# Optimization experiments

Measured on AMD Instinct MI355X. Metric: run time of the kernel, lower is better.

## Reference

```python
import jax, jax.numpy as jnp
import numpy as np
import math

IN_FEATURES = 4096
OUT_FEATURES = 4096
TOKENS = 8192


def hadamard(x):
    """Orthonormal fast Walsh-Hadamard transform along last dim (power of two)."""
    n = x.shape[-1]
    orig_shape = x.shape
    y = x.reshape(-1, n)
    h = 1
    while h < n:  # log2(n) butterfly steps (static loop, n known at trace time)
        y = y.reshape(-1, n // (2 * h), 2 * h)
        left = y[..., :h]
        right = y[..., h:2 * h]
        y = jnp.concatenate([left + right, left - right], axis=-1)
        y = y.reshape(-1, n)
        h *= 2
    return (y / math.sqrt(n)).reshape(orig_shape)


def setup_inputs() -> dict:
    key = jax.random.key(0)
    k1, k2, k3, k4 = jax.random.split(key, 4)
    x = jax.random.normal(k1, (TOKENS, IN_FEATURES), dtype=jnp.float32)
    # int8-valued quantized weights, stored as int32 for portability
    Q_tilde = jax.random.randint(k2, (OUT_FEATURES, IN_FEATURES), -127, 128, dtype=jnp.int32)
    # per-row scales, positive, realistic magnitude (~max_abs/127)
    s_tilde = jax.random.uniform(k3, (OUT_FEATURES, 1), dtype=jnp.float32, minval=0.001, maxval=0.02)
    bias = jax.random.normal(k4, (OUT_FEATURES,), dtype=jnp.float32)
    return {"x": x, "Q_tilde": Q_tilde, "s_tilde": s_tilde, "bias": bias}


def reference(x, Q_tilde, s_tilde, bias):
    # y = hadamard(x) @ (Q * s)^T + bias
    xh = hadamard(x)                                      # [T, in]
    W = Q_tilde.astype(jnp.float32) * s_tilde             # [out, in] dequantized
    y = xh @ W.T + bias                                   # [T, out]
    return y
```

## Files before the change

### kernel.cpp

```cpp
#include <hip/hip_runtime.h>
#include <hip/hip_bf16.h>

typedef int   i32x4 __attribute__((ext_vector_type(4)));
typedef unsigned int   u32;
typedef unsigned short u16;
typedef signed char    i8;

#define TOKENS 8192
#define NDIM   4096
#define KDIM   4096
#define BK     64
#define NKT    (KDIM / BK)

__global__ __launch_bounds__(64)
void fwht_rows_q8(const float* __restrict__ x, i8* __restrict__ xq,
                  float* __restrict__ xscale) {
  const int row = blockIdx.x;
  const int l   = threadIdx.x;

  const float4* xv = reinterpret_cast<const float4*>(x + (size_t)row * KDIM) + l * 16;
  float v[64];
#pragma unroll
  for (int j = 0; j < 16; ++j) {
    float4 f = xv[j];
    v[4*j+0] = f.x; v[4*j+1] = f.y; v[4*j+2] = f.z; v[4*j+3] = f.w;
  }

#pragma unroll
  for (int h = 1; h < 64; h <<= 1) {
#pragma unroll
    for (int j = 0; j < 64; ++j) {
      if ((j & h) == 0) {
        float a = v[j], b = v[j + h];
        v[j] = a + b; v[j + h] = a - b;
      }
    }
  }

#pragma unroll
  for (int m = 1; m < 64; m <<= 1) {
    const bool up = (l & m) != 0;
#pragma unroll
    for (int j = 0; j < 64; ++j) {
      float p = __shfl_xor(v[j], m, 64);
      v[j] = up ? (p - v[j]) : (v[j] + p);
    }
  }

  float mxu = 0.f;
#pragma unroll
  for (int j = 0; j < 64; ++j) mxu = fmaxf(mxu, fabsf(v[j]));
#pragma unroll
  for (int m = 1; m < 64; m <<= 1) mxu = fmaxf(mxu, __shfl_xor(mxu, m, 64));
  mxu = fmaxf(mxu, 1e-30f);
  const float inv = 127.0f / mxu;

  i8* orow = xq + (size_t)row * KDIM + l * 64;
#pragma unroll
  for (int g = 0; g < 4; ++g) {
    u32 w[4];
#pragma unroll
    for (int q4 = 0; q4 < 4; ++q4) {
      int b0 = __float2int_rn(v[g*16+q4*4+0] * inv);
      int b1 = __float2int_rn(v[g*16+q4*4+1] * inv);
      int b2 = __float2int_rn(v[g*16+q4*4+2] * inv);
      int b3 = __float2int_rn(v[g*16+q4*4+3] * inv);
      b0 = min(127, max(-127, b0)); b1 = min(127, max(-127, b1));
      b2 = min(127, max(-127, b2)); b3 = min(127, max(-127, b3));
      w[q4] = (u32)(b0 & 0xff) | ((u32)(b1 & 0xff) << 8) |
              ((u32)(b2 & 0xff) << 16) | ((u32)(b3 & 0xff) << 24);
    }
    uint4 pk; pk.x = w[0]; pk.y = w[1]; pk.z = w[2]; pk.w = w[3];
    *reinterpret_cast<uint4*>(orow + g * 16) = pk;
  }
  if (l == 0) xscale[row] = mxu * (0.015625f / 127.0f);
}

__device__ __forceinline__ u32 pack4(int4 q) {
  return (u32)(q.x & 0xff) | ((u32)(q.y & 0xff) << 8) |
         ((u32)(q.z & 0xff) << 16) | ((u32)(q.w & 0xff) << 24);
}
__global__ __launch_bounds__(256)
void qpack(const int* __restrict__ Q, i8* __restrict__ W8) {
  const size_t idx = ((size_t)blockIdx.x * 256 + threadIdx.x) * 16;
  int4 a = *reinterpret_cast<const int4*>(Q + idx);
  int4 b = *reinterpret_cast<const int4*>(Q + idx + 4);
  int4 c = *reinterpret_cast<const int4*>(Q + idx + 8);
  int4 d = *reinterpret_cast<const int4*>(Q + idx + 12);
  uint4 pk; pk.x = pack4(a); pk.y = pack4(b); pk.z = pack4(c); pk.w = pack4(d);
  *reinterpret_cast<uint4*>(W8 + idx) = pk;
}

__global__ __launch_bounds__(512, 4)
void gemm_i8_2b(const i8* __restrict__ A, const i8* __restrict__ B,
                const float* __restrict__ xscale, const float* __restrict__ s,
                const float* __restrict__ bias, float* __restrict__ C) {
  __shared__ __align__(16) i8 lds[2 * 24576];

  const int th   = threadIdx.x;
  const int wave = th >> 6;
  const int lane = th & 63;

  const int b0 = blockIdx.x;
  const int xc = b0 & 7;
  const int i  = b0 >> 3;
  const int mt = i >> 2;
  const int nt = xc * 4 + (i & 3);

  const int srow = th >> 2;
  const int scol = ((th & 3) * 16) ^ (((th >> 5) & 1) << 5);
  const i8* gA0 = A + (size_t)(mt * 256 + srow) * KDIM + scol;
  const i8* gA1 = gA0 + (size_t)128 * KDIM;
  const i8* gB0 = B + (size_t)(nt * 128 + srow) * KDIM + scol;

  const int ldsA0 = wave * 1024;
  const int ldsA1 = 8192 + wave * 1024;
  const int ldsB0 = 16384 + wave * 1024;

#define STAGE(tt, ss) do {                                                      \
    __builtin_amdgcn_global_load_lds(                                           \
      (const __attribute__((address_space(1))) void*)(gA0 + (size_t)(tt) * BK), \
      (__attribute__((address_space(3))) void*)(lds + (ss) * 24576 + ldsA0), 16, 0, 0); \
    __builtin_amdgcn_global_load_lds(                                           \
      (const __attribute__((address_space(1))) void*)(gA1 + (size_t)(tt) * BK), \
      (__attribute__((address_space(3))) void*)(lds + (ss) * 24576 + ldsA1), 16, 0, 0); \
    __builtin_amdgcn_global_load_lds(                                           \
      (const __attribute__((address_space(1))) void*)(gB0 + (size_t)(tt) * BK), \
      (__attribute__((address_space(3))) void*)(lds + (ss) * 24576 + ldsB0), 16, 0, 0); \
  } while (0)

  const int wm = wave >> 1;
  const int wn = wave & 1;
  const int laneRow = lane & 15;
  const int kByte   = (lane >> 4) << 4;
  const int swz     = ((lane >> 3) & 1) << 5;
  const int aOff = (((wm * 64 + laneRow) * 64 + kByte) ^ swz);
  const int bOff = (((wn * 64 + laneRow) * 64 + kByte) ^ swz) + 16384;

  i32x4 acc[4][4];
#pragma unroll
  for (int mi = 0; mi < 4; ++mi)
#pragma unroll
    for (int ni = 0; ni < 4; ++ni)
      acc[mi][ni] = i32x4{0, 0, 0, 0};

  STAGE(0, 0);
  asm volatile("s_waitcnt vmcnt(0)" ::: "memory");
  __builtin_amdgcn_s_barrier();

  for (int t = 0; t < NKT; ++t) {
    const char* cur = (const char*)lds + (t & 1) * 24576;
    if (t + 1 < NKT) STAGE(t + 1, (t + 1) & 1);

    i32x4 bfr[4], af[4];
#pragma unroll
    for (int ni = 0; ni < 4; ++ni)
      bfr[ni] = *(const i32x4*)(cur + bOff + ni * 1024);
#pragma unroll
    for (int mi = 0; mi < 4; ++mi)
      af[mi] = *(const i32x4*)(cur + aOff + mi * 1024);

    __builtin_amdgcn_s_setprio(1);
#pragma unroll
    for (int mi = 0; mi < 4; ++mi)
#pragma unroll
      for (int ni = 0; ni < 4; ++ni)
        acc[mi][ni] = __builtin_amdgcn_mfma_i32_16x16x64_i8(af[mi], bfr[ni], acc[mi][ni], 0, 0, 0);
    __builtin_amdgcn_s_setprio(0);

    asm volatile("s_waitcnt vmcnt(0)" ::: "memory");
    __builtin_amdgcn_s_barrier();
  }
#undef STAGE

  const int col0 = nt * 128 + wn * 64 + (lane & 15);
  const int row0 = mt * 256 + wm * 64 + ((lane >> 4) << 2);
  float xs[4][4];
#pragma unroll
  for (int mi = 0; mi < 4; ++mi)
#pragma unroll
    for (int r = 0; r < 4; ++r)
      xs[r][mi] = xscale[row0 + mi * 16 + r];
#pragma unroll
  for (int ni = 0; ni < 4; ++ni) {
    const float sc = s[col0 + ni * 16];
    const float bv = bias[col0 + ni * 16];
#pragma unroll
    for (int mi = 0; mi < 4; ++mi) {
      float* cp = C + (size_t)(row0 + mi * 16) * NDIM + col0 + ni * 16;
#pragma unroll
      for (int r = 0; r < 4; ++r)
        cp[(size_t)r * NDIM] = (float)acc[mi][ni][r] * (xs[r][mi] * sc) + bv;
    }
  }
}

extern "C" void kernel_launch(void* const* d_in, const int* in_sizes, int n_in,
                              void* d_out, int out_size, void* d_ws, size_t ws_size,
                              hipStream_t stream) {
  (void)in_sizes; (void)n_in; (void)out_size; (void)ws_size;
  const float* x    = (const float*)d_in[0];
  const int*   Q    = (const int*)d_in[1];
  const float* s    = (const float*)d_in[2];
  const float* bias = (const float*)d_in[3];
  float* out = (float*)d_out;

  i8*    xq     = (i8*)d_ws;
  i8*    W8     = xq + (size_t)TOKENS * KDIM;
  float* xscale = (float*)(W8 + (size_t)NDIM * KDIM);

  fwht_rows_q8<<<dim3(TOKENS), dim3(64), 0, stream>>>(x, xq, xscale);
  qpack<<<dim3((NDIM * KDIM) / (256 * 16)), dim3(256), 0, stream>>>(Q, W8);
  gemm_i8_2b<<<dim3((TOKENS / 256) * (NDIM / 128)), dim3(512), 0, stream>>>(
      xq, W8, xscale, s, bias, out);
}
```

Measured before the change: 219.4 us.

## Replace LDS-staged int8 GEMM with direct-to-register double-buffered loads on 256x256 tiles

The GEMM no longer stages tiles through shared memory. Each wave loads its A and B MFMA fragments straight from global memory into registers, using two register sets so the next K-step loads while the current one computes, and the kernel has no barriers. The block tile grows from 256x128 to 256x256 and each wave owns a 128x64 sub-tile, which raises register use and lowers the occupancy hint to 2. The cost is the loss of LDS data sharing between waves: each fragment is now fetched from global/L2 by several waves, and the per-lane 16-byte strided row loads may coalesce poorly.

Result: slower. 460.2 us (+109.8%).

```diff
diff --git a/kernel.cpp b/kernel.cpp
--- a/kernel.cpp
+++ b/kernel.cpp
@@ -91,12 +91,10 @@
   *reinterpret_cast<uint4*>(W8 + idx) = pk;
 }
 
-__global__ __launch_bounds__(512, 4)
-void gemm_i8_2b(const i8* __restrict__ A, const i8* __restrict__ B,
+__global__ __launch_bounds__(512, 2)
+void gemm_dr_i8(const i8* __restrict__ A, const i8* __restrict__ B,
                 const float* __restrict__ xscale, const float* __restrict__ s,
                 const float* __restrict__ bias, float* __restrict__ C) {
-  __shared__ __align__(16) i8 lds[2 * 24576];
-
   const int th   = threadIdx.x;
   const int wave = th >> 6;
   const int lane = th & 63;
@@ -104,80 +102,73 @@
   const int b0 = blockIdx.x;
   const int xc = b0 & 7;
   const int i  = b0 >> 3;
-  const int mt = i >> 2;
-  const int nt = xc * 4 + (i & 3);
-
-  const int srow = th >> 2;
-  const int scol = ((th & 3) * 16) ^ (((th >> 5) & 1) << 5);
-  const i8* gA0 = A + (size_t)(mt * 256 + srow) * KDIM + scol;
-  const i8* gA1 = gA0 + (size_t)128 * KDIM;
-  const i8* gB0 = B + (size_t)(nt * 128 + srow) * KDIM + scol;
-
-  const int ldsA0 = wave * 1024;
-  const int ldsA1 = 8192 + wave * 1024;
-  const int ldsB0 = 16384 + wave * 1024;
-
-#define STAGE(tt, ss) do {                                                      \
-    __builtin_amdgcn_global_load_lds(                                           \
-      (const __attribute__((address_space(1))) void*)(gA0 + (size_t)(tt) * BK), \
-      (__attribute__((address_space(3))) void*)(lds + (ss) * 24576 + ldsA0), 16, 0, 0); \
-    __builtin_amdgcn_global_load_lds(                                           \
-      (const __attribute__((address_space(1))) void*)(gA1 + (size_t)(tt) * BK), \
-      (__attribute__((address_space(3))) void*)(lds + (ss) * 24576 + ldsA1), 16, 0, 0); \
-    __builtin_amdgcn_global_load_lds(                                           \
-      (const __attribute__((address_space(1))) void*)(gB0 + (size_t)(tt) * BK), \
-      (__attribute__((address_space(3))) void*)(lds + (ss) * 24576 + ldsB0), 16, 0, 0); \
-  } while (0)
-
-  const int wm = wave >> 1;
-  const int wn = wave & 1;
+  const int mt = i >> 1;
+  const int nt = xc * 2 + (i & 1);
+
+  const int wm = wave >> 2;
+  const int wn = wave & 3;
   const int laneRow = lane & 15;
-  const int kByte   = (lane >> 4) << 4;
-  const int swz     = ((lane >> 3) & 1) << 5;
-  const int aOff = (((wm * 64 + laneRow) * 64 + kByte) ^ swz);
-  const int bOff = (((wn * 64 + laneRow) * 64 + kByte) ^ swz) + 16384;
-
-  i32x4 acc[4][4];
-#pragma unroll
-  for (int mi = 0; mi < 4; ++mi)
+  const int kB      = (lane >> 4) << 4;
+
+  u32 aoff[8], boff[4];
+#pragma unroll
+  for (int mi = 0; mi < 8; ++mi)
+    aoff[mi] = (u32)(mt * 256 + wm * 128 + mi * 16 + laneRow) * (u32)KDIM + (u32)kB;
+#pragma unroll
+  for (int ni = 0; ni < 4; ++ni)
+    boff[ni] = (u32)(nt * 256 + wn * 64 + ni * 16 + laneRow) * (u32)KDIM + (u32)kB;
+
+  i32x4 acc[8][4];
+#pragma unroll
+  for (int mi = 0; mi < 8; ++mi)
 #pragma unroll
     for (int ni = 0; ni < 4; ++ni)
       acc[mi][ni] = i32x4{0, 0, 0, 0};
 
-  STAGE(0, 0);
+  i32x4 a0[8], b0f[4], a1[8], b1f[4];
+
+#define LOADSET(as, bs, tt) do {                                        \
+    _Pragma("unroll")                                                   \
+    for (int mi = 0; mi < 8; ++mi)                                      \
+      as[mi] = *(const i32x4*)(A + aoff[mi] + (tt) * BK);               \
+    _Pragma("unroll")                                                   \
+    for (int ni = 0; ni < 4; ++ni)                                      \
+      bs[ni] = *(const i32x4*)(B + boff[ni] + (tt) * BK);               \
+  } while (0)
+
+#define MFMASET(as, bs) do {                                            \
+    _Pragma("unroll")                                                   \
+    for (int mi = 0; mi < 8; ++mi)                                      \
+      _Pragma("unroll")                                                 \
+      for (int ni = 0; ni < 4; ++ni)                                    \
+        acc[mi][ni] = __builtin_amdgcn_mfma_i32_16x16x64_i8(            \
+            as[mi], bs[ni], acc[mi][ni], 0, 0, 0);                      \
+  } while (0)
+
+  LOADSET(a0, b0f, 0);
+  LOADSET(a1, b1f, 1);
+
+  for (int t = 0; t < NKT - 2; t += 2) {
+    asm volatile("s_waitcnt vmcnt(12)" ::: "memory");
+    MFMASET(a0, b0f);
+    LOADSET(a0, b0f, t + 2);
+    asm volatile("s_waitcnt vmcnt(12)" ::: "memory");
+    MFMASET(a1, b1f);
+    LOADSET(a1, b1f, t + 3);
+  }
+  asm volatile("s_waitcnt vmcnt(12)" ::: "memory");
+  MFMASET(a0, b0f);
   asm volatile("s_waitcnt vmcnt(0)" ::: "memory");
-  __builtin_amdgcn_s_barrier();
-
-  for (int t = 0; t < NKT; ++t) {
-    const char* cur = (const char*)lds + (t & 1) * 24576;
-    if (t + 1 < NKT) STAGE(t + 1, (t + 1) & 1);
-
-    i32x4 bfr[4], af[4];
-#pragma unroll
-    for (int ni = 0; ni < 4; ++ni)
-      bfr[ni] = *(const i32x4*)(cur + bOff + ni * 1024);
-#pragma unroll
-    for (int mi = 0; mi < 4; ++mi)
-      af[mi] = *(const i32x4*)(cur + aOff + mi * 1024);
-
-    __builtin_amdgcn_s_setprio(1);
-#pragma unroll
-    for (int mi = 0; mi < 4; ++mi)
-#pragma unroll
-      for (int ni = 0; ni < 4; ++ni)
-        acc[mi][ni] = __builtin_amdgcn_mfma_i32_16x16x64_i8(af[mi], bfr[ni], acc[mi][ni], 0, 0, 0);
-    __builtin_amdgcn_s_setprio(0);
-
-    asm volatile("s_waitcnt vmcnt(0)" ::: "memory");
-    __builtin_amdgcn_s_barrier();
-  }
-#undef STAGE
-
-  const int col0 = nt * 128 + wn * 64 + (lane & 15);
-  const int row0 = mt * 256 + wm * 64 + ((lane >> 4) << 2);
-  float xs[4][4];
-#pragma unroll
-  for (int mi = 0; mi < 4; ++mi)
+  MFMASET(a1, b1f);
+
+#undef LOADSET
+#undef MFMASET
+
+  const int col0 = nt * 256 + wn * 64 + (lane & 15);
+  const int row0 = mt * 256 + wm * 128 + ((lane >> 4) << 2);
+  float xs[4][8];
+#pragma unroll
+  for (int mi = 0; mi < 8; ++mi)
 #pragma unroll
     for (int r = 0; r < 4; ++r)
       xs[r][mi] = xscale[row0 + mi * 16 + r];
@@ -186,7 +177,7 @@
     const float sc = s[col0 + ni * 16];
     const float bv = bias[col0 + ni * 16];
 #pragma unroll
-    for (int mi = 0; mi < 4; ++mi) {
+    for (int mi = 0; mi < 8; ++mi) {
       float* cp = C + (size_t)(row0 + mi * 16) * NDIM + col0 + ni * 16;
 #pragma unroll
       for (int r = 0; r < 4; ++r)
@@ -211,6 +202,6 @@
 
   fwht_rows_q8<<<dim3(TOKENS), dim3(64), 0, stream>>>(x, xq, xscale);
   qpack<<<dim3((NDIM * KDIM) / (256 * 16)), dim3(256), 0, stream>>>(Q, W8);
-  gemm_i8_2b<<<dim3((TOKENS / 256) * (NDIM / 128)), dim3(512), 0, stream>>>(
+  gemm_dr_i8<<<dim3((TOKENS / 256) * (NDIM / 256)), dim3(512), 0, stream>>>(
       xq, W8, xscale, s, bias, out);
 }
```

## Enlarge GEMM tile to 256x256 with triple-buffered LDS and fuse prep kernels

Applied to the files above, without the earlier changes.

The int8 GEMM moves from a 256x128 tile with 8 waves to a 256x256 tile with 4 waves. Each wave now holds an 8x8 grid of MFMA accumulators, and the K loop uses a three-slot LDS ring that prefetches two tiles ahead, with hand-placed waitcnt and sched barriers so LDS fragment loads overlap MFMAs. The FWHT/quantize and weight-pack kernels are merged into one launch to cut launch overhead. This raises arithmetic intensity and reduces barriers per MFMA, but heavy register pressure (256 accumulator registers) limits occupancy to one block per SIMD group and risks spills.

New measurement: 426.6 us. 94.5% more time.

```diff
diff --git a/kernel.cpp b/kernel.cpp
--- a/kernel.cpp
+++ b/kernel.cpp
@@ -11,12 +11,29 @@
 #define KDIM   4096
 #define BK     64
 #define NKT    (KDIM / BK)
-
-__global__ __launch_bounds__(64)
-void fwht_rows_q8(const float* __restrict__ x, i8* __restrict__ xq,
-                  float* __restrict__ xscale) {
-  const int row = blockIdx.x;
-  const int l   = threadIdx.x;
+#define SLOT   32768
+
+__device__ __forceinline__ u32 pack4(int4 q) {
+  return (u32)(q.x & 0xff) | ((u32)(q.y & 0xff) << 8) |
+         ((u32)(q.z & 0xff) << 16) | ((u32)(q.w & 0xff) << 24);
+}
+
+__global__ __launch_bounds__(256)
+void fused_aux(const float* __restrict__ x, i8* __restrict__ xq,
+               float* __restrict__ xscale,
+               const int* __restrict__ Q, i8* __restrict__ W8) {
+  if (blockIdx.x >= 2048) {
+    const size_t idx = (((size_t)(blockIdx.x - 2048)) * 256 + threadIdx.x) * 16;
+    int4 a = *reinterpret_cast<const int4*>(Q + idx);
+    int4 b = *reinterpret_cast<const int4*>(Q + idx + 4);
+    int4 c = *reinterpret_cast<const int4*>(Q + idx + 8);
+    int4 d = *reinterpret_cast<const int4*>(Q + idx + 12);
+    uint4 pk; pk.x = pack4(a); pk.y = pack4(b); pk.z = pack4(c); pk.w = pack4(d);
+    *reinterpret_cast<uint4*>(W8 + idx) = pk;
+    return;
+  }
+  const int row = blockIdx.x * 4 + (threadIdx.x >> 6);
+  const int l   = threadIdx.x & 63;
 
   const float4* xv = reinterpret_cast<const float4*>(x + (size_t)row * KDIM) + l * 16;
   float v[64];
@@ -76,26 +93,11 @@
   if (l == 0) xscale[row] = mxu * (0.015625f / 127.0f);
 }
 
-__device__ __forceinline__ u32 pack4(int4 q) {
-  return (u32)(q.x & 0xff) | ((u32)(q.y & 0xff) << 8) |
-         ((u32)(q.z & 0xff) << 16) | ((u32)(q.w & 0xff) << 24);
-}
-__global__ __launch_bounds__(256)
-void qpack(const int* __restrict__ Q, i8* __restrict__ W8) {
-  const size_t idx = ((size_t)blockIdx.x * 256 + threadIdx.x) * 16;
-  int4 a = *reinterpret_cast<const int4*>(Q + idx);
-  int4 b = *reinterpret_cast<const int4*>(Q + idx + 4);
-  int4 c = *reinterpret_cast<const int4*>(Q + idx + 8);
-  int4 d = *reinterpret_cast<const int4*>(Q + idx + 12);
-  uint4 pk; pk.x = pack4(a); pk.y = pack4(b); pk.z = pack4(c); pk.w = pack4(d);
-  *reinterpret_cast<uint4*>(W8 + idx) = pk;
-}
-
-__global__ __launch_bounds__(512, 4)
-void gemm_i8_2b(const i8* __restrict__ A, const i8* __restrict__ B,
-                const float* __restrict__ xscale, const float* __restrict__ s,
-                const float* __restrict__ bias, float* __restrict__ C) {
-  __shared__ __align__(16) i8 lds[2 * 24576];
+__global__ __launch_bounds__(256, 1)
+void gemm_w4(const i8* __restrict__ A, const i8* __restrict__ B,
+             const float* __restrict__ xscale, const float* __restrict__ s,
+             const float* __restrict__ bias, float* __restrict__ C) {
+  __shared__ __align__(16) i8 lds[3 * SLOT];
 
   const int th   = threadIdx.x;
   const int wave = th >> 6;
@@ -104,29 +106,30 @@
   const int b0 = blockIdx.x;
   const int xc = b0 & 7;
   const int i  = b0 >> 3;
-  const int mt = i >> 2;
-  const int nt = xc * 4 + (i & 3);
+  const int mt = i >> 1;
+  const int nt = xc * 2 + (i & 1);
 
   const int srow = th >> 2;
   const int scol = ((th & 3) * 16) ^ (((th >> 5) & 1) << 5);
-  const i8* gA0 = A + (size_t)(mt * 256 + srow) * KDIM + scol;
-  const i8* gA1 = gA0 + (size_t)128 * KDIM;
-  const i8* gB0 = B + (size_t)(nt * 128 + srow) * KDIM + scol;
-
-  const int ldsA0 = wave * 1024;
-  const int ldsA1 = 8192 + wave * 1024;
-  const int ldsB0 = 16384 + wave * 1024;
-
-#define STAGE(tt, ss) do {                                                      \
-    __builtin_amdgcn_global_load_lds(                                           \
-      (const __attribute__((address_space(1))) void*)(gA0 + (size_t)(tt) * BK), \
-      (__attribute__((address_space(3))) void*)(lds + (ss) * 24576 + ldsA0), 16, 0, 0); \
-    __builtin_amdgcn_global_load_lds(                                           \
-      (const __attribute__((address_space(1))) void*)(gA1 + (size_t)(tt) * BK), \
-      (__attribute__((address_space(3))) void*)(lds + (ss) * 24576 + ldsA1), 16, 0, 0); \
-    __builtin_amdgcn_global_load_lds(                                           \
-      (const __attribute__((address_space(1))) void*)(gB0 + (size_t)(tt) * BK), \
-      (__attribute__((address_space(3))) void*)(lds + (ss) * 24576 + ldsB0), 16, 0, 0); \
+  const i8* gA[4]; const i8* gB[4];
+#pragma unroll
+  for (int j = 0; j < 4; ++j) {
+    gA[j] = A + (size_t)(mt * 256 + j * 64 + srow) * KDIM + scol;
+    gB[j] = B + (size_t)(nt * 256 + j * 64 + srow) * KDIM + scol;
+  }
+  const int ldsW = wave * 1024;
+
+#define STAGE(tt, ss) do {                                                        \
+    _Pragma("unroll")                                                             \
+    for (int j = 0; j < 4; ++j)                                                   \
+      __builtin_amdgcn_global_load_lds(                                           \
+        (const __attribute__((address_space(1))) void*)(gA[j] + (size_t)(tt) * BK), \
+        (__attribute__((address_space(3))) void*)(lds + (ss) * SLOT + j * 4096 + ldsW), 16, 0, 0); \
+    _Pragma("unroll")                                                             \
+    for (int j = 0; j < 4; ++j)                                                   \
+      __builtin_amdgcn_global_load_lds(                                           \
+        (const __attribute__((address_space(1))) void*)(gB[j] + (size_t)(tt) * BK), \
+        (__attribute__((address_space(3))) void*)(lds + (ss) * SLOT + 16384 + j * 4096 + ldsW), 16, 0, 0); \
   } while (0)
 
   const int wm = wave >> 1;
@@ -134,59 +137,101 @@
   const int laneRow = lane & 15;
   const int kByte   = (lane >> 4) << 4;
   const int swz     = ((lane >> 3) & 1) << 5;
-  const int aOff = (((wm * 64 + laneRow) * 64 + kByte) ^ swz);
-  const int bOff = (((wn * 64 + laneRow) * 64 + kByte) ^ swz) + 16384;
-
-  i32x4 acc[4][4];
-#pragma unroll
-  for (int mi = 0; mi < 4; ++mi)
-#pragma unroll
-    for (int ni = 0; ni < 4; ++ni)
+  const int aOff = (((wm * 128 + laneRow) * 64 + kByte) ^ swz);
+  const int bOff = (((wn * 128 + laneRow) * 64 + kByte) ^ swz) + 16384;
+
+  i32x4 acc[8][8];
+#pragma unroll
+  for (int mi = 0; mi < 8; ++mi)
+#pragma unroll
+    for (int ni = 0; ni < 8; ++ni)
       acc[mi][ni] = i32x4{0, 0, 0, 0};
 
+  i32x4 afA[4], afB[4], bf0[8], bf1[8];
+
   STAGE(0, 0);
-  asm volatile("s_waitcnt vmcnt(0)" ::: "memory");
+  STAGE(1, 1);
+  asm volatile("s_waitcnt vmcnt(8)" ::: "memory");
+  __builtin_amdgcn_sched_barrier(0);
   __builtin_amdgcn_s_barrier();
-
-  for (int t = 0; t < NKT; ++t) {
-    const char* cur = (const char*)lds + (t & 1) * 24576;
-    if (t + 1 < NKT) STAGE(t + 1, (t + 1) & 1);
-
-    i32x4 bfr[4], af[4];
-#pragma unroll
-    for (int ni = 0; ni < 4; ++ni)
-      bfr[ni] = *(const i32x4*)(cur + bOff + ni * 1024);
+  {
+    const char* c0 = (const char*)lds;
+#pragma unroll
+    for (int ni = 0; ni < 8; ++ni)
+      bf0[ni] = *(const i32x4*)(c0 + bOff + ni * 1024);
 #pragma unroll
     for (int mi = 0; mi < 4; ++mi)
-      af[mi] = *(const i32x4*)(cur + aOff + mi * 1024);
-
-    __builtin_amdgcn_s_setprio(1);
-#pragma unroll
-    for (int mi = 0; mi < 4; ++mi)
-#pragma unroll
-      for (int ni = 0; ni < 4; ++ni)
-        acc[mi][ni] = __builtin_amdgcn_mfma_i32_16x16x64_i8(af[mi], bfr[ni], acc[mi][ni], 0, 0, 0);
-    __builtin_amdgcn_s_setprio(0);
-
-    asm volatile("s_waitcnt vmcnt(0)" ::: "memory");
-    __builtin_amdgcn_s_barrier();
-  }
+      afA[mi] = *(const i32x4*)(c0 + aOff + mi * 1024);
+  }
+
+  int sCur = 0, sNxt = 1, sStg = 2;
+
+#define TILE(t, BFC, BFN) do {                                                    \
+    const char* cur = (const char*)lds + sCur * SLOT;                             \
+    const char* nxt = (const char*)lds + sNxt * SLOT;                             \
+    _Pragma("unroll")                                                             \
+    for (int mi = 0; mi < 4; ++mi)                                                \
+      afB[mi] = *(const i32x4*)(cur + aOff + 4096 + mi * 1024);                   \
+    if ((t) + 2 < NKT) STAGE((t) + 2, sStg);                                      \
+    asm volatile("s_waitcnt lgkmcnt(4)" ::: "memory");       \
+    __builtin_amdgcn_sched_barrier(0);                                            \
+    __builtin_amdgcn_s_setprio(1);                                                \
+    _Pragma("unroll")                                                             \
+    for (int mi = 0; mi < 4; ++mi)                                                \
+      _Pragma("unroll")                                                           \
+      for (int ni = 0; ni < 8; ++ni)                                              \
+        acc[mi][ni] = __builtin_amdgcn_mfma_i32_16x16x64_i8(afA[mi], BFC[ni],     \
+                                                            acc[mi][ni], 0, 0, 0); \
+    __builtin_amdgcn_s_setprio(0);                                                \
+    if ((t) + 2 < NKT)      { asm volatile("s_waitcnt vmcnt(8)" ::: "memory"); }  \
+    else if ((t) + 1 < NKT) { asm volatile("s_waitcnt vmcnt(0)" ::: "memory"); }  \
+    __builtin_amdgcn_sched_barrier(0);                                            \
+    if ((t) + 1 < NKT) {                                                          \
+      __builtin_amdgcn_s_barrier();      \
+      _Pragma("unroll")                                                           \
+      for (int ni = 0; ni < 8; ++ni)                                              \
+        BFN[ni] = *(const i32x4*)(nxt + bOff + ni * 1024);                        \
+      _Pragma("unroll")                                                           \
+      for (int mi = 0; mi < 4; ++mi)                                              \
+        afA[mi] = *(const i32x4*)(nxt + aOff + mi * 1024);                        \
+      asm volatile("s_waitcnt lgkmcnt(12)" ::: "memory");          \
+      __builtin_amdgcn_sched_barrier(0);                                          \
+    } else {                                                                      \
+      asm volatile("s_waitcnt lgkmcnt(0)" ::: "memory");                          \
+      __builtin_amdgcn_sched_barrier(0);                                          \
+    }                                                                             \
+    __builtin_amdgcn_s_setprio(1);                                                \
+    _Pragma("unroll")                                                             \
+    for (int mi = 0; mi < 4; ++mi)                                                \
+      _Pragma("unroll")                                                           \
+      for (int ni = 0; ni < 8; ++ni)                                              \
+        acc[mi + 4][ni] = __builtin_amdgcn_mfma_i32_16x16x64_i8(afB[mi], BFC[ni], \
+                                                        acc[mi + 4][ni], 0, 0, 0); \
+    __builtin_amdgcn_s_setprio(0);                                                \
+    int _tmp = sCur; sCur = sNxt; sNxt = sStg; sStg = _tmp;                       \
+  } while (0)
+
+  for (int t = 0; t < NKT; t += 2) {
+    TILE(t,     bf0, bf1);
+    TILE(t + 1, bf1, bf0);
+  }
+#undef TILE
 #undef STAGE
 
-  const int col0 = nt * 128 + wn * 64 + (lane & 15);
-  const int row0 = mt * 256 + wm * 64 + ((lane >> 4) << 2);
-  float xs[4][4];
-#pragma unroll
-  for (int mi = 0; mi < 4; ++mi)
+  const int col0 = nt * 256 + wn * 128 + (lane & 15);
+  const int row0 = mt * 256 + wm * 128 + ((lane >> 4) << 2);
+  float xs[4][8];
+#pragma unroll
+  for (int mi = 0; mi < 8; ++mi)
 #pragma unroll
     for (int r = 0; r < 4; ++r)
       xs[r][mi] = xscale[row0 + mi * 16 + r];
 #pragma unroll
-  for (int ni = 0; ni < 4; ++ni) {
+  for (int ni = 0; ni < 8; ++ni) {
     const float sc = s[col0 + ni * 16];
     const float bv = bias[col0 + ni * 16];
 #pragma unroll
-    for (int mi = 0; mi < 4; ++mi) {
+    for (int mi = 0; mi < 8; ++mi) {
       float* cp = C + (size_t)(row0 + mi * 16) * NDIM + col0 + ni * 16;
 #pragma unroll
       for (int r = 0; r < 4; ++r)
@@ -209,8 +254,7 @@
   i8*    W8     = xq + (size_t)TOKENS * KDIM;
   float* xscale = (float*)(W8 + (size_t)NDIM * KDIM);
 
-  fwht_rows_q8<<<dim3(TOKENS), dim3(64), 0, stream>>>(x, xq, xscale);
-  qpack<<<dim3((NDIM * KDIM) / (256 * 16)), dim3(256), 0, stream>>>(Q, W8);
-  gemm_i8_2b<<<dim3((TOKENS / 256) * (NDIM / 128)), dim3(512), 0, stream>>>(
+  fused_aux<<<dim3(6144), dim3(256), 0, stream>>>(x, xq, xscale, Q, W8);
+  gemm_w4<<<dim3((TOKENS / 256) * (NDIM / 256)), dim3(256), 0, stream>>>(
       xq, W8, xscale, s, bias, out);
 }
```

## Fuse FWHT and weight packing into one launch; use 4-wave GEMM with 128x64 wave tiles

Applied to the files above, without the earlier changes.

The FWHT-quantize and int32-to-int8 weight packing kernels become one launch, with block ranges split by blockIdx, and the FWHT packs four rows into each 256-thread block. The GEMM keeps its 256x128 block tile but drops from 8 waves to 4. Each wave now computes a 128x64 sub-tile with 8x4 MFMA accumulators, which raises register reuse of the B fragments and cuts LDS reads per MFMA. The cost is higher register pressure (launch bounds 256,2), fewer waves to hide latency, and more global-to-LDS loads per thread per stage.

After: 201.8 us. 1.09x faster.

```diff
diff --git a/kernel.cpp b/kernel.cpp
--- a/kernel.cpp
+++ b/kernel.cpp
@@ -11,12 +11,29 @@
 #define KDIM   4096
 #define BK     64
 #define NKT    (KDIM / BK)
-
-__global__ __launch_bounds__(64)
-void fwht_rows_q8(const float* __restrict__ x, i8* __restrict__ xq,
-                  float* __restrict__ xscale) {
-  const int row = blockIdx.x;
-  const int l   = threadIdx.x;
+#define SLOT   24576
+
+__device__ __forceinline__ u32 pack4(int4 q) {
+  return (u32)(q.x & 0xff) | ((u32)(q.y & 0xff) << 8) |
+         ((u32)(q.z & 0xff) << 16) | ((u32)(q.w & 0xff) << 24);
+}
+
+__global__ __launch_bounds__(256)
+void fused_aux(const float* __restrict__ x, i8* __restrict__ xq,
+               float* __restrict__ xscale,
+               const int* __restrict__ Q, i8* __restrict__ W8) {
+  if (blockIdx.x >= 2048) {
+    const size_t idx = (((size_t)(blockIdx.x - 2048)) * 256 + threadIdx.x) * 16;
+    int4 a = *reinterpret_cast<const int4*>(Q + idx);
+    int4 b = *reinterpret_cast<const int4*>(Q + idx + 4);
+    int4 c = *reinterpret_cast<const int4*>(Q + idx + 8);
+    int4 d = *reinterpret_cast<const int4*>(Q + idx + 12);
+    uint4 pk; pk.x = pack4(a); pk.y = pack4(b); pk.z = pack4(c); pk.w = pack4(d);
+    *reinterpret_cast<uint4*>(W8 + idx) = pk;
+    return;
+  }
+  const int row = blockIdx.x * 4 + (threadIdx.x >> 6);
+  const int l   = threadIdx.x & 63;
 
   const float4* xv = reinterpret_cast<const float4*>(x + (size_t)row * KDIM) + l * 16;
   float v[64];
@@ -76,26 +93,11 @@
   if (l == 0) xscale[row] = mxu * (0.015625f / 127.0f);
 }
 
-__device__ __forceinline__ u32 pack4(int4 q) {
-  return (u32)(q.x & 0xff) | ((u32)(q.y & 0xff) << 8) |
-         ((u32)(q.z & 0xff) << 16) | ((u32)(q.w & 0xff) << 24);
-}
-__global__ __launch_bounds__(256)
-void qpack(const int* __restrict__ Q, i8* __restrict__ W8) {
-  const size_t idx = ((size_t)blockIdx.x * 256 + threadIdx.x) * 16;
-  int4 a = *reinterpret_cast<const int4*>(Q + idx);
-  int4 b = *reinterpret_cast<const int4*>(Q + idx + 4);
-  int4 c = *reinterpret_cast<const int4*>(Q + idx + 8);
-  int4 d = *reinterpret_cast<const int4*>(Q + idx + 12);
-  uint4 pk; pk.x = pack4(a); pk.y = pack4(b); pk.z = pack4(c); pk.w = pack4(d);
-  *reinterpret_cast<uint4*>(W8 + idx) = pk;
-}
-
-__global__ __launch_bounds__(512, 4)
-void gemm_i8_2b(const i8* __restrict__ A, const i8* __restrict__ B,
-                const float* __restrict__ xscale, const float* __restrict__ s,
-                const float* __restrict__ bias, float* __restrict__ C) {
-  __shared__ __align__(16) i8 lds[2 * 24576];
+__global__ __launch_bounds__(256, 2)
+void gemm_2x4(const i8* __restrict__ A, const i8* __restrict__ B,
+              const float* __restrict__ xscale, const float* __restrict__ s,
+              const float* __restrict__ bias, float* __restrict__ C) {
+  __shared__ __align__(16) i8 lds[2 * SLOT];
 
   const int th   = threadIdx.x;
   const int wave = th >> 6;
@@ -109,24 +111,26 @@
 
   const int srow = th >> 2;
   const int scol = ((th & 3) * 16) ^ (((th >> 5) & 1) << 5);
-  const i8* gA0 = A + (size_t)(mt * 256 + srow) * KDIM + scol;
-  const i8* gA1 = gA0 + (size_t)128 * KDIM;
-  const i8* gB0 = B + (size_t)(nt * 128 + srow) * KDIM + scol;
-
-  const int ldsA0 = wave * 1024;
-  const int ldsA1 = 8192 + wave * 1024;
-  const int ldsB0 = 16384 + wave * 1024;
-
-#define STAGE(tt, ss) do {                                                      \
-    __builtin_amdgcn_global_load_lds(                                           \
-      (const __attribute__((address_space(1))) void*)(gA0 + (size_t)(tt) * BK), \
-      (__attribute__((address_space(3))) void*)(lds + (ss) * 24576 + ldsA0), 16, 0, 0); \
-    __builtin_amdgcn_global_load_lds(                                           \
-      (const __attribute__((address_space(1))) void*)(gA1 + (size_t)(tt) * BK), \
-      (__attribute__((address_space(3))) void*)(lds + (ss) * 24576 + ldsA1), 16, 0, 0); \
-    __builtin_amdgcn_global_load_lds(                                           \
-      (const __attribute__((address_space(1))) void*)(gB0 + (size_t)(tt) * BK), \
-      (__attribute__((address_space(3))) void*)(lds + (ss) * 24576 + ldsB0), 16, 0, 0); \
+  const i8* gA[4]; const i8* gB[2];
+#pragma unroll
+  for (int j = 0; j < 4; ++j)
+    gA[j] = A + (size_t)(mt * 256 + j * 64 + srow) * KDIM + scol;
+#pragma unroll
+  for (int j = 0; j < 2; ++j)
+    gB[j] = B + (size_t)(nt * 128 + j * 64 + srow) * KDIM + scol;
+  const int ldsW = wave * 1024;
+
+#define STAGE(tt, ss) do {                                                        \
+    _Pragma("unroll")                                                             \
+    for (int j = 0; j < 4; ++j)                                                   \
+      __builtin_amdgcn_global_load_lds(                                           \
+        (const __attribute__((address_space(1))) void*)(gA[j] + (size_t)(tt) * BK), \
+        (__attribute__((address_space(3))) void*)(lds + (ss) * SLOT + j * 4096 + ldsW), 16, 0, 0); \
+    _Pragma("unroll")                                                             \
+    for (int j = 0; j < 2; ++j)                                                   \
+      __builtin_amdgcn_global_load_lds(                                           \
+        (const __attribute__((address_space(1))) void*)(gB[j] + (size_t)(tt) * BK), \
+        (__attribute__((address_space(3))) void*)(lds + (ss) * SLOT + 16384 + j * 4096 + ldsW), 16, 0, 0); \
   } while (0)
 
   const int wm = wave >> 1;
@@ -134,12 +138,12 @@
   const int laneRow = lane & 15;
   const int kByte   = (lane >> 4) << 4;
   const int swz     = ((lane >> 3) & 1) << 5;
-  const int aOff = (((wm * 64 + laneRow) * 64 + kByte) ^ swz);
+  const int aOff = (((wm * 128 + laneRow) * 64 + kByte) ^ swz);
   const int bOff = (((wn * 64 + laneRow) * 64 + kByte) ^ swz) + 16384;
 
-  i32x4 acc[4][4];
-#pragma unroll
-  for (int mi = 0; mi < 4; ++mi)
+  i32x4 acc[8][4];
+#pragma unroll
+  for (int mi = 0; mi < 8; ++mi)
 #pragma unroll
     for (int ni = 0; ni < 4; ++ni)
       acc[mi][ni] = i32x4{0, 0, 0, 0};
@@ -149,20 +153,20 @@
   __builtin_amdgcn_s_barrier();
 
   for (int t = 0; t < NKT; ++t) {
-    const char* cur = (const char*)lds + (t & 1) * 24576;
+    const char* cur = (const char*)lds + (t & 1) * SLOT;
     if (t + 1 < NKT) STAGE(t + 1, (t + 1) & 1);
 
-    i32x4 bfr[4], af[4];
+    i32x4 bfr[4], af[8];
 #pragma unroll
     for (int ni = 0; ni < 4; ++ni)
       bfr[ni] = *(const i32x4*)(cur + bOff + ni * 1024);
 #pragma unroll
-    for (int mi = 0; mi < 4; ++mi)
+    for (int mi = 0; mi < 8; ++mi)
       af[mi] = *(const i32x4*)(cur + aOff + mi * 1024);
 
     __builtin_amdgcn_s_setprio(1);
 #pragma unroll
-    for (int mi = 0; mi < 4; ++mi)
+    for (int mi = 0; mi < 8; ++mi)
 #pragma unroll
       for (int ni = 0; ni < 4; ++ni)
         acc[mi][ni] = __builtin_amdgcn_mfma_i32_16x16x64_i8(af[mi], bfr[ni], acc[mi][ni], 0, 0, 0);
@@ -174,10 +178,10 @@
 #undef STAGE
 
   const int col0 = nt * 128 + wn * 64 + (lane & 15);
-  const int row0 = mt * 256 + wm * 64 + ((lane >> 4) << 2);
-  float xs[4][4];
-#pragma unroll
-  for (int mi = 0; mi < 4; ++mi)
+  const int row0 = mt * 256 + wm * 128 + ((lane >> 4) << 2);
+  float xs[4][8];
+#pragma unroll
+  for (int mi = 0; mi < 8; ++mi)
 #pragma unroll
     for (int r = 0; r < 4; ++r)
       xs[r][mi] = xscale[row0 + mi * 16 + r];
@@ -186,7 +190,7 @@
     const float sc = s[col0 + ni * 16];
     const float bv = bias[col0 + ni * 16];
 #pragma unroll
-    for (int mi = 0; mi < 4; ++mi) {
+    for (int mi = 0; mi < 8; ++mi) {
       float* cp = C + (size_t)(row0 + mi * 16) * NDIM + col0 + ni * 16;
 #pragma unroll
       for (int r = 0; r < 4; ++r)
@@ -209,8 +213,7 @@
   i8*    W8     = xq + (size_t)TOKENS * KDIM;
   float* xscale = (float*)(W8 + (size_t)NDIM * KDIM);
 
-  fwht_rows_q8<<<dim3(TOKENS), dim3(64), 0, stream>>>(x, xq, xscale);
-  qpack<<<dim3((NDIM * KDIM) / (256 * 16)), dim3(256), 0, stream>>>(Q, W8);
-  gemm_i8_2b<<<dim3((TOKENS / 256) * (NDIM / 128)), dim3(512), 0, stream>>>(
+  fused_aux<<<dim3(6144), dim3(256), 0, stream>>>(x, xq, xscale, Q, W8);
+  gemm_2x4<<<dim3((TOKENS / 256) * (NDIM / 128)), dim3(256), 0, stream>>>(
       xq, W8, xscale, s, bias, out);
 }
```
